# Performance work log

Measured on AMD Instinct MI355X. Metric: run time of the kernel, lower is better.

The kernel has to match this reference:

```python
import jax, jax.numpy as jnp
import numpy as np

CELLS = 512

def setup_inputs() -> dict:
    key = jax.random.key(0)
    ks = jax.random.split(key, 9)
    B, T, C, L = 256, 8192, 32, 16
    classes = 10
    def g(k, shape, fan_in):
        return jax.random.normal(k, shape, dtype=jnp.float32) * (1.0 / np.sqrt(fan_in))
    return {
        "x": jax.random.normal(ks[0], (B, T, C), dtype=jnp.float32),
        "W0": g(ks[1], (C, L, 1, 32), L),
        "b0": g(ks[2], (C, 32), 32),
        "W1": g(ks[3], (C, 1, 32, 32), 32),
        "b1": g(ks[4], (C, 32), 32),
        "W2": g(ks[5], (C, 1, 32, 16), 32),
        "b2": g(ks[6], (C, 16), 16),
        "Wf": g(ks[7], (C, 1, 16, classes), 16),
        "bf": jnp.zeros((C, classes), dtype=jnp.float32),
    }

def reference(x, W0, b0, W1, b1, W2, b2, Wf, bf):
    B, T, C = x.shape
    L = T // CELLS
    # per-cell min-max midpoint normalization
    xc = x.reshape(B, CELLS, L, C)
    mid = (jnp.min(xc, axis=2) + jnp.max(xc, axis=2)) * 0.5  # [B, cells, C]
    norm = xc - mid[:, :, None, :]  # [B, cells, L, C]
    # first conv: width=L, stride=L, VALID  ==  per-cell dense over L
    h = jax.nn.relu(jnp.einsum('bslc,clk->bsck', norm, W0[:, :, 0, :]) + b0)  # [B, cells, C, 32]
    # width-1 convs == pointwise dense per channel
    h = jax.nn.relu(jnp.einsum('bsck,ckm->bscm', h, W1[:, 0]) + b1)
    h = jax.nn.relu(jnp.einsum('bsck,ckm->bscm', h, W2[:, 0]) + b2)
    logits = jnp.einsum('bsck,cko->bsco', h, Wf[:, 0]) + bf  # [B, cells, C, classes]
    probs = jax.nn.softmax(logits, axis=-1)
    # concat over channels along last axis -> [B, cells, C*classes]
    return probs.reshape(B, CELLS, -1)
```

## Files before the change

kernel.cpp:

```cpp
#include <hip/hip_runtime.h>


#define THREADS 512
#define CPG     8
#define TILE_U  64
#define TPB     32
#define WSTRIDE 2304
#define XSTRIDE 145
#define LDS_FLOATS (CPG * WSTRIDE + TILE_U * XSTRIDE)

__global__ __launch_bounds__(THREADS, 2)
void shapelet_kernel(const float* __restrict__ x,
                     const float* __restrict__ W0, const float* __restrict__ b0,
                     const float* __restrict__ W1, const float* __restrict__ b1,
                     const float* __restrict__ W2, const float* __restrict__ b2,
                     const float* __restrict__ Wf, const float* __restrict__ bf,
                     float* __restrict__ out)
{
    extern __shared__ float lds[];
    float* wlds = lds;
    float* lx   = lds + CPG * WSTRIDE;

    const int tid     = threadIdx.x;
    const int lane    = tid & 63;
    const int wv      = tid >> 6;
    const int g       = blockIdx.x & 3;
    const int tstream = blockIdx.x >> 2;

    {
        const int c = g * CPG + wv;
        float* wd = wlds + wv * WSTRIDE;
        const float* s0 = W0 + c * 512;
        for (int i = lane; i < 512; i += 64) wd[i] = s0[i];
        if (lane < 32) wd[512 + lane] = b0[c * 32 + lane];
        const float* s1 = W1 + c * 1024;
        for (int i = lane; i < 1024; i += 64) wd[544 + i] = s1[i];
        if (lane < 32) wd[1568 + lane] = b1[c * 32 + lane];
        const float* s2 = W2 + c * 512;
        for (int i = lane; i < 512; i += 64) wd[1600 + i] = s2[i];
        if (lane < 16) wd[2112 + lane] = b2[c * 16 + lane];
        const float* sf = Wf + c * 160;
        for (int i = lane; i < 160; i += 64) {
            int k = i / 10, o = i - k * 10;
            wd[2128 + o * 16 + k] = sf[i];
        }
        if (lane < 10) wd[2288 + lane] = bf[c * 10 + lane];
    }

    const float4* xg = reinterpret_cast<const float4*>(x);
    float4 pre[4];
    {
        size_t unit0 = (size_t)(tstream * TPB) * TILE_U;
        #pragma unroll
        for (int it = 0; it < 4; ++it) {
            int m = it * THREADS + tid;
            int uu = m >> 5, l = (m >> 1) & 15, q = m & 1;
            pre[it] = xg[(unit0 + uu) * 128 + l * 8 + g * 2 + q];
        }
    }

    const int cw = wv;
    const float* wb = wlds + cw * WSTRIDE;
    const int u = lane;

    for (int j = 0; j < TPB; ++j) {
        const int tile  = tstream * TPB + j;
        const int unit0 = tile * TILE_U;

        __syncthreads();
        #pragma unroll
        for (int it = 0; it < 4; ++it) {
            int m = it * THREADS + tid;
            int uu = m >> 5, l = (m >> 1) & 15, q = m & 1;
            float* d = lx + uu * XSTRIDE + l * 9 + q * 4;
            d[0] = pre[it].x; d[1] = pre[it].y; d[2] = pre[it].z; d[3] = pre[it].w;
        }
        __syncthreads();

        if (j + 1 < TPB) {
            size_t unit0n = (size_t)(unit0 + TILE_U);
            #pragma unroll
            for (int it = 0; it < 4; ++it) {
                int m = it * THREADS + tid;
                int uu = m >> 5, l = (m >> 1) & 15, q = m & 1;
                pre[it] = xg[(unit0n + uu) * 128 + l * 8 + g * 2 + q];
            }
        }

        float xx[16];
        #pragma unroll
        for (int l = 0; l < 16; ++l)
            xx[l] = lx[u * XSTRIDE + l * 9 + cw];

        float mn = xx[0], mx = xx[0];
        #pragma unroll
        for (int l = 1; l < 16; ++l) {
            mn = fminf(mn, xx[l]);
            mx = fmaxf(mx, xx[l]);
        }
        const float mid = 0.5f * (mn + mx);
        #pragma unroll
        for (int l = 0; l < 16; ++l) xx[l] -= mid;

        float h0[32];
        #pragma unroll
        for (int k4 = 0; k4 < 8; ++k4) {
            float4 bb = *reinterpret_cast<const float4*>(wb + 512 + k4 * 4);
            h0[k4*4+0] = bb.x; h0[k4*4+1] = bb.y; h0[k4*4+2] = bb.z; h0[k4*4+3] = bb.w;
        }
        #pragma unroll
        for (int l = 0; l < 16; ++l) {
            const float xv = xx[l];
            #pragma unroll
            for (int k4 = 0; k4 < 8; ++k4) {
                float4 w = *reinterpret_cast<const float4*>(wb + l * 32 + k4 * 4);
                h0[k4*4+0] = fmaf(xv, w.x, h0[k4*4+0]);
                h0[k4*4+1] = fmaf(xv, w.y, h0[k4*4+1]);
                h0[k4*4+2] = fmaf(xv, w.z, h0[k4*4+2]);
                h0[k4*4+3] = fmaf(xv, w.w, h0[k4*4+3]);
            }
        }
        #pragma unroll
        for (int k = 0; k < 32; ++k) h0[k] = fmaxf(h0[k], 0.0f);

        float h1[32];
        #pragma unroll
        for (int m4 = 0; m4 < 8; ++m4) {
            float4 bb = *reinterpret_cast<const float4*>(wb + 1568 + m4 * 4);
            h1[m4*4+0] = bb.x; h1[m4*4+1] = bb.y; h1[m4*4+2] = bb.z; h1[m4*4+3] = bb.w;
        }
        #pragma unroll
        for (int k = 0; k < 32; ++k) {
            const float hv = h0[k];
            #pragma unroll
            for (int m4 = 0; m4 < 8; ++m4) {
                float4 w = *reinterpret_cast<const float4*>(wb + 544 + k * 32 + m4 * 4);
                h1[m4*4+0] = fmaf(hv, w.x, h1[m4*4+0]);
                h1[m4*4+1] = fmaf(hv, w.y, h1[m4*4+1]);
                h1[m4*4+2] = fmaf(hv, w.z, h1[m4*4+2]);
                h1[m4*4+3] = fmaf(hv, w.w, h1[m4*4+3]);
            }
        }
        #pragma unroll
        for (int k = 0; k < 32; ++k) h1[k] = fmaxf(h1[k], 0.0f);

        float h2[16];
        #pragma unroll
        for (int j4 = 0; j4 < 4; ++j4) {
            float4 bb = *reinterpret_cast<const float4*>(wb + 2112 + j4 * 4);
            h2[j4*4+0] = bb.x; h2[j4*4+1] = bb.y; h2[j4*4+2] = bb.z; h2[j4*4+3] = bb.w;
        }
        #pragma unroll
        for (int k = 0; k < 32; ++k) {
            const float hv = h1[k];
            #pragma unroll
            for (int j4 = 0; j4 < 4; ++j4) {
                float4 w = *reinterpret_cast<const float4*>(wb + 1600 + k * 16 + j4 * 4);
                h2[j4*4+0] = fmaf(hv, w.x, h2[j4*4+0]);
                h2[j4*4+1] = fmaf(hv, w.y, h2[j4*4+1]);
                h2[j4*4+2] = fmaf(hv, w.z, h2[j4*4+2]);
                h2[j4*4+3] = fmaf(hv, w.w, h2[j4*4+3]);
            }
        }
        #pragma unroll
        for (int k = 0; k < 16; ++k) h2[k] = fmaxf(h2[k], 0.0f);

        float lg[10];
        #pragma unroll
        for (int o = 0; o < 10; ++o) {
            float acc = wb[2288 + o];
            #pragma unroll
            for (int k4 = 0; k4 < 4; ++k4) {
                float4 w = *reinterpret_cast<const float4*>(wb + 2128 + o * 16 + k4 * 4);
                acc = fmaf(h2[k4*4+0], w.x, acc);
                acc = fmaf(h2[k4*4+1], w.y, acc);
                acc = fmaf(h2[k4*4+2], w.z, acc);
                acc = fmaf(h2[k4*4+3], w.w, acc);
            }
            lg[o] = acc;
        }

        float mxl = lg[0];
        #pragma unroll
        for (int o = 1; o < 10; ++o) mxl = fmaxf(mxl, lg[o]);
        float s = 0.0f;
        #pragma unroll
        for (int o = 0; o < 10; ++o) {
            lg[o] = __expf(lg[o] - mxl);
            s += lg[o];
        }
        const float r = 1.0f / s;

        float2* op = reinterpret_cast<float2*>(
            out + (size_t)(unit0 + u) * 320 + (g * CPG + cw) * 10);
        #pragma unroll
        for (int o = 0; o < 5; ++o)
            op[o] = make_float2(lg[2*o] * r, lg[2*o+1] * r);
    }
}

extern "C" void kernel_launch(void* const* d_in, const int* in_sizes, int n_in,
                              void* d_out, int out_size, void* d_ws, size_t ws_size,
                              hipStream_t stream) {
    const float* x  = (const float*)d_in[0];
    const float* W0 = (const float*)d_in[1];
    const float* b0 = (const float*)d_in[2];
    const float* W1 = (const float*)d_in[3];
    const float* b1 = (const float*)d_in[4];
    const float* W2 = (const float*)d_in[5];
    const float* b2 = (const float*)d_in[6];
    const float* Wf = (const float*)d_in[7];
    const float* bf = (const float*)d_in[8];
    float* out = (float*)d_out;

    const size_t shmem = LDS_FLOATS * sizeof(float);
    hipFuncSetAttribute((const void*)shapelet_kernel,
                        hipFuncAttributeMaxDynamicSharedMemorySize, (int)shmem);

    shapelet_kernel<<<dim3(256), dim3(THREADS), shmem, stream>>>(
        x, W0, b0, W1, b1, W2, b2, Wf, bf, out);
}
```

Baseline: 731.2 us.

## Double block size to share LDS weights across two unit halves, remap blocks per XCD

Blocks now have 1024 threads covering 128 units per tile, so each copy of the per-channel weights in LDS serves twice as many units and the weight preload is split across both wave halves. Block indices are remapped so that the four channel-group blocks of a unit stream run on the same XCD, which lets them share x reads in L2. Occupancy is pinned with amdgpu_waves_per_eu(4,4) in place of launch bounds. The larger block raises LDS per block and sets a tighter register budget, which could cause spills or lower residency.

```diff
diff --git a/kernel.cpp b/kernel.cpp
--- a/kernel.cpp
+++ b/kernel.cpp
@@ -1,15 +1,15 @@
 #include <hip/hip_runtime.h>
 
 
-#define THREADS 512
+#define THREADS 1024
 #define CPG     8
-#define TILE_U  64
-#define TPB     32
+#define TILE_U  128
+#define TPB     16
 #define WSTRIDE 2304
 #define XSTRIDE 145
 #define LDS_FLOATS (CPG * WSTRIDE + TILE_U * XSTRIDE)
 
-__global__ __launch_bounds__(THREADS, 2)
+__global__ __attribute__((amdgpu_waves_per_eu(4, 4)))
 void shapelet_kernel(const float* __restrict__ x,
                      const float* __restrict__ W0, const float* __restrict__ b0,
                      const float* __restrict__ W1, const float* __restrict__ b1,
@@ -21,58 +21,68 @@
     float* wlds = lds;
     float* lx   = lds + CPG * WSTRIDE;
 
-    const int tid     = threadIdx.x;
-    const int lane    = tid & 63;
-    const int wv      = tid >> 6;
-    const int g       = blockIdx.x & 3;
-    const int tstream = blockIdx.x >> 2;
+    const int tid  = threadIdx.x;
+    const int lane = tid & 63;
+    const int wv   = tid >> 6;
+    const int cw   = wv & 7;
+    const int uh   = wv >> 3;
+
+    const int bid     = blockIdx.x;
+    const int xcd     = bid & 7;
+    const int r       = bid >> 3;
+    const int g       = r & 3;
+    const int q       = r >> 2;
+    const int ustream = xcd * 8 + q;
 
     {
-        const int c = g * CPG + wv;
-        float* wd = wlds + wv * WSTRIDE;
+        const int c = g * CPG + cw;
+        float* wd = wlds + cw * WSTRIDE;
+        const int i0 = lane + uh * 64;
         const float* s0 = W0 + c * 512;
-        for (int i = lane; i < 512; i += 64) wd[i] = s0[i];
-        if (lane < 32) wd[512 + lane] = b0[c * 32 + lane];
+        for (int i = i0; i < 512; i += 128) wd[i] = s0[i];
         const float* s1 = W1 + c * 1024;
-        for (int i = lane; i < 1024; i += 64) wd[544 + i] = s1[i];
-        if (lane < 32) wd[1568 + lane] = b1[c * 32 + lane];
+        for (int i = i0; i < 1024; i += 128) wd[544 + i] = s1[i];
         const float* s2 = W2 + c * 512;
-        for (int i = lane; i < 512; i += 64) wd[1600 + i] = s2[i];
-        if (lane < 16) wd[2112 + lane] = b2[c * 16 + lane];
+        for (int i = i0; i < 512; i += 128) wd[1600 + i] = s2[i];
         const float* sf = Wf + c * 160;
-        for (int i = lane; i < 160; i += 64) {
+        for (int i = i0; i < 160; i += 128) {
             int k = i / 10, o = i - k * 10;
             wd[2128 + o * 16 + k] = sf[i];
         }
-        if (lane < 10) wd[2288 + lane] = bf[c * 10 + lane];
+        if (uh == 0) {
+            if (lane < 32) wd[512  + lane] = b0[c * 32 + lane];
+            if (lane < 32) wd[1568 + lane] = b1[c * 32 + lane];
+        } else {
+            if (lane < 16) wd[2112 + lane] = b2[c * 16 + lane];
+            if (lane < 10) wd[2288 + lane] = bf[c * 10 + lane];
+        }
     }
 
     const float4* xg = reinterpret_cast<const float4*>(x);
     float4 pre[4];
     {
-        size_t unit0 = (size_t)(tstream * TPB) * TILE_U;
+        size_t unit0 = (size_t)(ustream * TPB) * TILE_U;
         #pragma unroll
         for (int it = 0; it < 4; ++it) {
             int m = it * THREADS + tid;
-            int uu = m >> 5, l = (m >> 1) & 15, q = m & 1;
-            pre[it] = xg[(unit0 + uu) * 128 + l * 8 + g * 2 + q];
+            int uu = m >> 5, l = (m >> 1) & 15, qq = m & 1;
+            pre[it] = xg[(unit0 + uu) * 128 + l * 8 + g * 2 + qq];
         }
     }
 
-    const int cw = wv;
     const float* wb = wlds + cw * WSTRIDE;
-    const int u = lane;
-
+    const int u = lane + uh * 64;
+
+    #pragma unroll 1
     for (int j = 0; j < TPB; ++j) {
-        const int tile  = tstream * TPB + j;
-        const int unit0 = tile * TILE_U;
+        const int unit0 = (ustream * TPB + j) * TILE_U;
 
         __syncthreads();
         #pragma unroll
         for (int it = 0; it < 4; ++it) {
             int m = it * THREADS + tid;
-            int uu = m >> 5, l = (m >> 1) & 15, q = m & 1;
-            float* d = lx + uu * XSTRIDE + l * 9 + q * 4;
+            int uu = m >> 5, l = (m >> 1) & 15, qq = m & 1;
+            float* d = lx + uu * XSTRIDE + l * 9 + qq * 4;
             d[0] = pre[it].x; d[1] = pre[it].y; d[2] = pre[it].z; d[3] = pre[it].w;
         }
         __syncthreads();
@@ -82,8 +92,8 @@
             #pragma unroll
             for (int it = 0; it < 4; ++it) {
                 int m = it * THREADS + tid;
-                int uu = m >> 5, l = (m >> 1) & 15, q = m & 1;
-                pre[it] = xg[(unit0n + uu) * 128 + l * 8 + g * 2 + q];
+                int uu = m >> 5, l = (m >> 1) & 15, qq = m & 1;
+                pre[it] = xg[(unit0n + uu) * 128 + l * 8 + g * 2 + qq];
             }
         }
 
@@ -189,13 +199,13 @@
             lg[o] = __expf(lg[o] - mxl);
             s += lg[o];
         }
-        const float r = 1.0f / s;
+        const float rr = 1.0f / s;
 
         float2* op = reinterpret_cast<float2*>(
             out + (size_t)(unit0 + u) * 320 + (g * CPG + cw) * 10);
         #pragma unroll
         for (int o = 0; o < 5; ++o)
-            op[o] = make_float2(lg[2*o] * r, lg[2*o+1] * r);
+            op[o] = make_float2(lg[2*o] * rr, lg[2*o+1] * rr);
     }
 }
 
```

Result: faster. 636.4 us (-13.0%).
